# Optimization experiments

Measured on AMD Instinct MI355X. Metric: run time of the kernel, lower is better.

The kernel has to match this reference:

```python
import jax, jax.numpy as jnp
import numpy as np

D_MODEL = 1024
NUM_HEADS = 16
D_HEAD = D_MODEL // NUM_HEADS
THETA = 10000.0


def setup_inputs() -> dict:
    key = jax.random.key(0)
    ks = jax.random.split(key, 5)
    B, S = 2, 2048
    std = np.sqrt(2.0 / (D_MODEL + D_MODEL))
    return {
        "x": jax.random.normal(ks[0], (B, S, D_MODEL), dtype=jnp.float32),
        "token_positions": jnp.arange(S, dtype=jnp.int32),
        "wq": jax.random.normal(ks[1], (D_MODEL, D_MODEL), dtype=jnp.float32) * std,
        "wk": jax.random.normal(ks[2], (D_MODEL, D_MODEL), dtype=jnp.float32) * std,
        "wv": jax.random.normal(ks[3], (D_MODEL, D_MODEL), dtype=jnp.float32) * std,
        "wo": jax.random.normal(ks[4], (D_MODEL, D_MODEL), dtype=jnp.float32) * std,
    }


def _rope(x, token_positions):
    # x: [B, H, S, D_HEAD]; token_positions: [S]
    freq_idx = jnp.arange(0, D_HEAD, 2, dtype=jnp.float32)
    inv_freq = THETA ** (-freq_idx / D_HEAD)                      # [D_HEAD/2]
    angles = token_positions.astype(jnp.float32)[:, None] * inv_freq  # [S, D_HEAD/2]
    cos = jnp.cos(angles)[None, None, :, :]
    sin = jnp.sin(angles)[None, None, :, :]
    x_even = x[..., 0::2]
    x_odd = x[..., 1::2]
    rot_even = x_even * cos - x_odd * sin
    rot_odd = x_even * sin + x_odd * cos
    # interleave pairs back: [..., pairs, 2] -> [..., D_HEAD]
    return jnp.stack((rot_even, rot_odd), axis=-1).reshape(x.shape)


def reference(x, token_positions, wq, wk, wv, wo):
    B, S, _ = x.shape
    def proj(w):
        y = jnp.einsum('bsi,oi->bso', x, w)
        return y.reshape(B, S, NUM_HEADS, D_HEAD).transpose(0, 2, 1, 3)  # [B,H,S,Dh]
    q = _rope(proj(wq), token_positions)
    k = _rope(proj(wk), token_positions)
    v = proj(wv)
    scores = jnp.einsum('bhqd,bhkd->bhqk', q, k) / jnp.sqrt(jnp.float32(D_HEAD))
    causal = jnp.tril(jnp.ones((S, S), dtype=bool))
    scores = jnp.where(causal, scores, -jnp.inf)
    probs = jax.nn.softmax(scores, axis=-1)
    attn = jnp.einsum('bhqk,bhkd->bhqd', probs, v)
    attn = attn.transpose(0, 2, 1, 3).reshape(B, S, D_MODEL)
    return jnp.einsum('bsi,oi->bso', attn, wo)
```

## Files before the change

### kernel.cpp

```cpp
#include <hip/hip_runtime.h>
#include <math.h>

#define D_MODEL 1024
#define NUM_HEADS 16
#define D_HEAD 64
#define SEQ 2048
#define BATCH 2

typedef __attribute__((ext_vector_type(8))) short short8;
typedef __attribute__((ext_vector_type(4))) float float4v;

__device__ __forceinline__ short f2bf(float f) {
    unsigned u = __float_as_uint(f);
    u += 0x7FFFu + ((u >> 16) & 1u);
    return (short)(u >> 16);
}

__global__ __launch_bounds__(256) void cvt_bf16_kernel(
    const float* __restrict__ x,  const float* __restrict__ wq,
    const float* __restrict__ wk, const float* __restrict__ wv,
    const float* __restrict__ wo, const int* __restrict__ pos,
    short* __restrict__ xb,  short* __restrict__ wqb,
    short* __restrict__ wkb, short* __restrict__ wvb,
    short* __restrict__ wob,
    float* __restrict__ costab, float* __restrict__ sintab)
{
    const int a = blockIdx.y;
    if (a == 5) {
        const int idx = blockIdx.x * 256 + threadIdx.x;
        if (idx < SEQ * 32) {
            const int s = idx >> 5, fi = idx & 31;
            const float p = (float)pos[s];
            const float inv_freq = exp2f((float)fi * -0.4152410118609203f);
            float sn, cs;
            sincosf(p * inv_freq, &sn, &cs);
            costab[idx] = cs;
            sintab[idx] = sn;
        }
        return;
    }
    const float* src = (a == 0) ? x : (a == 1) ? wq : (a == 2) ? wk : (a == 3) ? wv : wo;
    short* dst = (a == 0) ? xb : (a == 1) ? wqb : (a == 2) ? wkb : (a == 3) ? wvb : wob;
    const int n = (a == 0) ? (BATCH * SEQ * D_MODEL) : (D_MODEL * D_MODEL);
    const int i = (blockIdx.x * 256 + threadIdx.x) * 8;
    if (i >= n) return;
    const float4 v0 = *(const float4*)(src + i);
    const float4 v1 = *(const float4*)(src + i + 4);
    short8 r;
    r[0] = f2bf(v0.x); r[1] = f2bf(v0.y); r[2] = f2bf(v0.z); r[3] = f2bf(v0.w);
    r[4] = f2bf(v1.x); r[5] = f2bf(v1.y); r[6] = f2bf(v1.z); r[7] = f2bf(v1.w);
    *(short8*)(dst + i) = r;
}

__device__ __forceinline__ void gemm_core_db(
    const short* __restrict__ a, const short* __restrict__ b,
    short* smem, int m0, int n0, float4v acc[4][4])
{
    const int tid = threadIdx.x;
    const int lane = tid & 63;
    const int l15 = lane & 15, quad = lane >> 4;
    const int wave = tid >> 6;
    const int mw = (wave & 1) * 64, nw = (wave >> 1) * 64;
    const int srow = tid >> 2;
    const int scol = (tid & 3) * 8;

    const short* ag = a + (size_t)(m0 + srow) * D_MODEL + scol;
    const short* bg = b + (size_t)(n0 + srow) * D_MODEL + scol;

    short* bufA[2] = { smem,        smem + 8192 };
    short* bufB[2] = { smem + 4096, smem + 12288 };

    short8 ga0 = *(const short8*)(ag);
    short8 ga1 = *(const short8*)(ag + (size_t)64 * D_MODEL);
    short8 gb0 = *(const short8*)(bg);
    short8 gb1 = *(const short8*)(bg + (size_t)64 * D_MODEL);
    *(short8*)&bufA[0][srow * 32 + scol]        = ga0;
    *(short8*)&bufA[0][(64 + srow) * 32 + scol] = ga1;
    *(short8*)&bufB[0][srow * 32 + scol]        = gb0;
    *(short8*)&bufB[0][(64 + srow) * 32 + scol] = gb1;
    ga0 = *(const short8*)(ag + 32);
    ga1 = *(const short8*)(ag + 32 + (size_t)64 * D_MODEL);
    gb0 = *(const short8*)(bg + 32);
    gb1 = *(const short8*)(bg + 32 + (size_t)64 * D_MODEL);

    for (int k = 0; k < 32; k++) {
        __syncthreads();
        if (k + 1 < 32) {
            short* bA = bufA[(k + 1) & 1];
            short* bB = bufB[(k + 1) & 1];
            *(short8*)&bA[srow * 32 + scol]        = ga0;
            *(short8*)&bA[(64 + srow) * 32 + scol] = ga1;
            *(short8*)&bB[srow * 32 + scol]        = gb0;
            *(short8*)&bB[(64 + srow) * 32 + scol] = gb1;
        }
        if (k + 2 < 32) {
            const int off = (k + 2) * 32;
            ga0 = *(const short8*)(ag + off);
            ga1 = *(const short8*)(ag + off + (size_t)64 * D_MODEL);
            gb0 = *(const short8*)(bg + off);
            gb1 = *(const short8*)(bg + off + (size_t)64 * D_MODEL);
        }
        const short* lA = bufA[k & 1];
        const short* lB = bufB[k & 1];
        short8 af[4], bf[4];
        #pragma unroll
        for (int i = 0; i < 4; i++)
            af[i] = *(const short8*)&lA[(mw + i * 16 + l15) * 32 + quad * 8];
        #pragma unroll
        for (int i = 0; i < 4; i++)
            bf[i] = *(const short8*)&lB[(nw + i * 16 + l15) * 32 + quad * 8];
        #pragma unroll
        for (int mi = 0; mi < 4; mi++)
            #pragma unroll
            for (int ni = 0; ni < 4; ni++)
                acc[mi][ni] = __builtin_amdgcn_mfma_f32_16x16x32_bf16(
                    af[mi], bf[ni], acc[mi][ni], 0, 0, 0);
    }
}

__global__ __launch_bounds__(256) void qk_mfma_kernel(
    const short* __restrict__ xb, const short* __restrict__ w,
    const float* __restrict__ costab, const float* __restrict__ sintab,
    short* __restrict__ dst, const float qs)
{
    __shared__ __align__(16) short smem[128 * 136];

    const int bid = blockIdx.x;
    const int m0 = (bid & 31) * 128;
    const int n0 = (bid >> 5) * 128;

    float4v acc[4][4];
    #pragma unroll
    for (int i = 0; i < 4; i++)
        #pragma unroll
        for (int j = 0; j < 4; j++)
            acc[i][j] = (float4v){0.f, 0.f, 0.f, 0.f};

    gemm_core_db(xb, w, smem, m0, n0, acc);

    const int tid = threadIdx.x;
    const int lane = tid & 63;
    const int l15 = lane & 15, quad = lane >> 4;
    const int wave = tid >> 6;
    const int mw = (wave & 1) * 64, nw = (wave >> 1) * 64;

    const int s_base = m0 & (SEQ - 1);
    const int bb = m0 >> 11;

    __syncthreads();

    #pragma unroll
    for (int ni = 0; ni < 4; ni++) {
        const int n = n0 + nw + ni * 16 + l15;
        const int d = n & 63;
        const int fi = d >> 1;
        #pragma unroll
        for (int mi = 0; mi < 4; mi++) {
            #pragma unroll
            for (int r = 0; r < 4; r++) {
                const int mloc = mw + mi * 16 + quad * 4 + r;
                const int ti = ((s_base + mloc) << 5) + fi;
                const float cs = costab[ti];
                const float sn = sintab[ti];
                const float val = acc[mi][ni][r];
                const float partner = __shfl_xor(val, 1, 64);
                const float res = (l15 & 1) ? fmaf(partner, sn, val * cs)
                                            : fmaf(val, cs, -partner * sn);
                smem[mloc * 136 + nw + ni * 16 + l15] = f2bf(res * qs);
            }
        }
    }
    __syncthreads();
    #pragma unroll
    for (int it = 0; it < 8; it++) {
        const int ri = it * 32 + (tid >> 3);
        const int mloc = ri & 127;
        const int hh = ri >> 7;
        const int nloc = hh * 64 + (tid & 7) * 8;
        const short8 val = *(const short8*)&smem[mloc * 136 + nloc];
        const int n = n0 + nloc;
        const int h = n >> 6, d = n & 63;
        *(short8*)(dst + ((size_t)(bb * NUM_HEADS + h) * SEQ + s_base + mloc) *
                   D_HEAD + d) = val;
    }
}

__global__ __launch_bounds__(256) void v_mfma_kernel(
    const short* __restrict__ xb, const short* __restrict__ w,
    short* __restrict__ Vt)
{
    __shared__ __align__(16) short smem[128 * 136];

    const int bid = blockIdx.x;
    const int m0 = (bid & 31) * 128;
    const int n0 = (bid >> 5) * 128;

    float4v acc[4][4];
    #pragma unroll
    for (int i = 0; i < 4; i++)
        #pragma unroll
        for (int j = 0; j < 4; j++)
            acc[i][j] = (float4v){0.f, 0.f, 0.f, 0.f};

    gemm_core_db(xb, w, smem, m0, n0, acc);

    const int tid = threadIdx.x;
    const int lane = tid & 63;
    const int l15 = lane & 15, quad = lane >> 4;
    const int wave = tid >> 6;
    const int mw = (wave & 1) * 64, nw = (wave >> 1) * 64;

    const int s_base = m0 & (SEQ - 1);
    const int bb = m0 >> 11;

    __syncthreads();
    #pragma unroll
    for (int ni = 0; ni < 4; ni++) {
        #pragma unroll
        for (int mi = 0; mi < 4; mi++) {
            #pragma unroll
            for (int r = 0; r < 4; r++)
                smem[(nw + ni * 16 + l15) * 136 + mw + mi * 16 + quad * 4 + r] =
                    f2bf(acc[mi][ni][r]);
        }
    }
    __syncthreads();
    #pragma unroll
    for (int it = 0; it < 8; it++) {
        const int nloc = it * 16 + (tid >> 4);
        const int mloc = (tid & 15) * 8;
        const short8 val = *(const short8*)&smem[nloc * 136 + mloc];
        const int n = n0 + nloc;
        const int h = n >> 6, d = n & 63;
        *(short8*)(Vt + ((size_t)(bb * NUM_HEADS + h) * D_HEAD + d) * SEQ +
                   s_base + mloc) = val;
    }
}

__global__ __launch_bounds__(256) void attn_mfma_kernel(
    const short* __restrict__ Qb, const short* __restrict__ Kb,
    const short* __restrict__ Vt, short* __restrict__ Ab)
{
    __shared__ __align__(16) short lK[32 * 72];
    __shared__ __align__(16) short lV[64 * 56];
    __shared__ __align__(16) short lP[4][16 * 56];

    const int tid = threadIdx.x;
    const int lane = tid & 63;
    const int wave = tid >> 6;
    const int l15 = lane & 15;
    const int quad = lane >> 4;

    const int bh = blockIdx.x & (BATCH * NUM_HEADS - 1);
    const int qt = (SEQ / 64 - 1) - (blockIdx.x >> 5);
    const int q0w = qt * 64 + wave * 16;

    const short* Kg = Kb + (size_t)bh * SEQ * D_HEAD;
    const short* Vg = Vt + (size_t)bh * D_HEAD * SEQ;

    const short* Qrow = Qb + ((size_t)bh * SEQ + q0w + l15) * D_HEAD;
    const short8 qf0 = *(const short8*)(Qrow + quad * 8);
    const short8 qf1 = *(const short8*)(Qrow + 32 + quad * 8);

    float4v o0 = {0.f, 0.f, 0.f, 0.f}, o1 = o0, o2 = o0, o3 = o0;
    float lp[4] = {0.f, 0.f, 0.f, 0.f};

    const int nt = qt * 2 + 2;
    const int krow = tid & 31, kch = tid >> 5;
    const int vrow = tid >> 2, vch = tid & 3;

    short8 kreg = *(const short8*)(Kg + (size_t)krow * D_HEAD + kch * 8);
    short8 vreg = *(const short8*)(Vg + (size_t)vrow * SEQ + vch * 8);

    for (int t = 0; t < nt; t++) {
        const int kt0 = t * 32;
        __syncthreads();
        *(short8*)&lK[krow * 72 + kch * 8] = kreg;
        *(short8*)&lV[vrow * 56 + vch * 8] = vreg;
        __syncthreads();
        if (t + 1 < nt) {
            kreg = *(const short8*)(Kg + (size_t)(kt0 + 32 + krow) * D_HEAD + kch * 8);
            vreg = *(const short8*)(Vg + (size_t)vrow * SEQ + kt0 + 32 + vch * 8);
        }
        if (kt0 > q0w + 15) continue;

        float4v s0 = {0.f, 0.f, 0.f, 0.f}, s1 = {0.f, 0.f, 0.f, 0.f};
        {
            const short8 b00 = *(const short8*)&lK[l15 * 72 + quad * 8];
            const short8 b10 = *(const short8*)&lK[(16 + l15) * 72 + quad * 8];
            s0 = __builtin_amdgcn_mfma_f32_16x16x32_bf16(qf0, b00, s0, 0, 0, 0);
            s1 = __builtin_amdgcn_mfma_f32_16x16x32_bf16(qf0, b10, s1, 0, 0, 0);
            const short8 b01 = *(const short8*)&lK[l15 * 72 + 32 + quad * 8];
            const short8 b11 = *(const short8*)&lK[(16 + l15) * 72 + 32 + quad * 8];
            s0 = __builtin_amdgcn_mfma_f32_16x16x32_bf16(qf1, b01, s0, 0, 0, 0);
            s1 = __builtin_amdgcn_mfma_f32_16x16x32_bf16(qf1, b11, s1, 0, 0, 0);
        }

        if (kt0 + 31 > q0w) {
            const int qbase = q0w + quad * 4;
            #pragma unroll
            for (int r = 0; r < 4; r++) {
                if (kt0 + l15 > qbase + r)      s0[r] = -INFINITY;
                if (kt0 + 16 + l15 > qbase + r) s1[r] = -INFINITY;
            }
        }

        float p0[4], p1[4];
        #pragma unroll
        for (int r = 0; r < 4; r++) {
            p0[r] = __expf(s0[r]);
            p1[r] = __expf(s1[r]);
            lp[r] += p0[r] + p1[r];
        }

        short* Pw = lP[wave];
        #pragma unroll
        for (int r = 0; r < 4; r++) {
            Pw[(quad * 4 + r) * 56 + l15]      = f2bf(p0[r]);
            Pw[(quad * 4 + r) * 56 + 16 + l15] = f2bf(p1[r]);
        }
        const short8 pa = *(const short8*)&lP[wave][l15 * 56 + quad * 8];

        const short8 v0 = *(const short8*)&lV[(0 * 16 + l15) * 56 + quad * 8];
        const short8 v1 = *(const short8*)&lV[(1 * 16 + l15) * 56 + quad * 8];
        const short8 v2 = *(const short8*)&lV[(2 * 16 + l15) * 56 + quad * 8];
        const short8 v3 = *(const short8*)&lV[(3 * 16 + l15) * 56 + quad * 8];
        o0 = __builtin_amdgcn_mfma_f32_16x16x32_bf16(pa, v0, o0, 0, 0, 0);
        o1 = __builtin_amdgcn_mfma_f32_16x16x32_bf16(pa, v1, o1, 0, 0, 0);
        o2 = __builtin_amdgcn_mfma_f32_16x16x32_bf16(pa, v2, o2, 0, 0, 0);
        o3 = __builtin_amdgcn_mfma_f32_16x16x32_bf16(pa, v3, o3, 0, 0, 0);
    }

    #pragma unroll
    for (int off = 1; off <= 8; off <<= 1) {
        #pragma unroll
        for (int r = 0; r < 4; r++) lp[r] += __shfl_xor(lp[r], off, 64);
    }

    const int b = bh >> 4, h = bh & 15;
    short* Ap = Ab + ((size_t)(b * SEQ) + q0w + quad * 4) * D_MODEL + h * D_HEAD;
    #pragma unroll
    for (int r = 0; r < 4; r++) {
        const float inv = 1.0f / lp[r];
        Ap[(size_t)r * D_MODEL + l15]      = f2bf(o0[r] * inv);
        Ap[(size_t)r * D_MODEL + 16 + l15] = f2bf(o1[r] * inv);
        Ap[(size_t)r * D_MODEL + 32 + l15] = f2bf(o2[r] * inv);
        Ap[(size_t)r * D_MODEL + 48 + l15] = f2bf(o3[r] * inv);
    }
}

__global__ __launch_bounds__(256) void out_mfma_kernel(
    const short* __restrict__ Ab, const short* __restrict__ wob,
    float* __restrict__ out)
{
    __shared__ __align__(16) short smem[2 * 8192];

    const int bid = blockIdx.x;
    const int m0 = (bid & 31) * 128;
    const int n0 = (bid >> 5) * 128;

    float4v acc[4][4];
    #pragma unroll
    for (int i = 0; i < 4; i++)
        #pragma unroll
        for (int j = 0; j < 4; j++)
            acc[i][j] = (float4v){0.f, 0.f, 0.f, 0.f};

    gemm_core_db(Ab, wob, smem, m0, n0, acc);

    const int tid = threadIdx.x;
    const int lane = tid & 63;
    const int l15 = lane & 15, quad = lane >> 4;
    const int wave = tid >> 6;
    const int mw = (wave & 1) * 64, nw = (wave >> 1) * 64;

    #pragma unroll
    for (int mi = 0; mi < 4; mi++) {
        #pragma unroll
        for (int r = 0; r < 4; r++) {
            const int m = m0 + mw + mi * 16 + quad * 4 + r;
            float* op = out + (size_t)m * D_MODEL + n0 + nw + l15;
            #pragma unroll
            for (int ni = 0; ni < 4; ni++)
                op[ni * 16] = acc[mi][ni][r];
        }
    }
}

extern "C" void kernel_launch(void* const* d_in, const int* in_sizes, int n_in,
                              void* d_out, int out_size, void* d_ws, size_t ws_size,
                              hipStream_t stream)
{
    const float* x  = (const float*)d_in[0];
    const int*  pos = (const int*)d_in[1];
    const float* wq = (const float*)d_in[2];
    const float* wk = (const float*)d_in[3];
    const float* wv = (const float*)d_in[4];
    const float* wo = (const float*)d_in[5];
    float* out = (float*)d_out;

    const size_t nx = (size_t)BATCH * SEQ * D_MODEL;
    const size_t nw = (size_t)D_MODEL * D_MODEL;
    short* xb  = (short*)d_ws;
    short* wqb = xb + nx;
    short* wkb = wqb + nw;
    short* wvb = wkb + nw;
    short* wob = wvb + nw;
    short* Qb  = wob + nw;
    short* Kb  = Qb + nx;
    short* Vt  = Kb + nx;
    short* Ab  = Vt + nx;
    float* costab = (float*)(Ab + nx);
    float* sintab = costab + SEQ * 32;

    dim3 blk(256);
    cvt_bf16_kernel<<<dim3(2048, 6), blk, 0, stream>>>(x, wq, wk, wv, wo, pos,
                                                       xb, wqb, wkb, wvb, wob,
                                                       costab, sintab);
    qk_mfma_kernel<<<dim3(256), blk, 0, stream>>>(xb, wqb, costab, sintab, Qb, 0.125f);
    qk_mfma_kernel<<<dim3(256), blk, 0, stream>>>(xb, wkb, costab, sintab, Kb, 1.0f);
    v_mfma_kernel<<<dim3(256), blk, 0, stream>>>(xb, wvb, Vt);
    attn_mfma_kernel<<<dim3(BATCH * NUM_HEADS * (SEQ / 64)), blk, 0, stream>>>(Qb, Kb, Vt, Ab);
    out_mfma_kernel<<<dim3(256), blk, 0, stream>>>(Ab, wob, out);
}
```

Before: 213.1 us.

## Merge Q/K/V projections into one launch and widen attention key tiles to 64

The three projection launches (Q, K with RoPE; V transposed) become a single 768-block kernel that picks its weight and epilogue by block index. This removes launch gaps and fills the GPU better than three 256-block grids. The attention kernel now processes 64 keys per iteration instead of 32 and computes S transposed (K as the A operand), so each lane owns one query row. That lets it keep a single running row sum, write P as packed 4-short stores and apply the causal mask through a predicated exp. The cost is more shared memory per block and more work per iteration on diagonal tiles, since whole 64-key tiles are processed even when partly masked.

```diff
diff --git a/kernel.cpp b/kernel.cpp
--- a/kernel.cpp
+++ b/kernel.cpp
@@ -8,6 +8,7 @@
 #define BATCH 2
 
 typedef __attribute__((ext_vector_type(8))) short short8;
+typedef __attribute__((ext_vector_type(4))) short short4v;
 typedef __attribute__((ext_vector_type(4))) float float4v;
 
 __device__ __forceinline__ short f2bf(float f) {
@@ -118,16 +119,19 @@
     }
 }
 
-__global__ __launch_bounds__(256) void qk_mfma_kernel(
-    const short* __restrict__ xb, const short* __restrict__ w,
+__global__ __launch_bounds__(256) void qkv_mfma_kernel(
+    const short* __restrict__ xb, const short* __restrict__ wqb,
+    const short* __restrict__ wkb, const short* __restrict__ wvb,
     const float* __restrict__ costab, const float* __restrict__ sintab,
-    short* __restrict__ dst, const float qs)
+    short* __restrict__ Qb, short* __restrict__ Kb, short* __restrict__ Vt)
 {
     __shared__ __align__(16) short smem[128 * 136];
 
-    const int bid = blockIdx.x;
+    const int z = blockIdx.x >> 8;
+    const int bid = blockIdx.x & 255;
     const int m0 = (bid & 31) * 128;
     const int n0 = (bid >> 5) * 128;
+    const short* w = (z == 0) ? wqb : (z == 1) ? wkb : wvb;
 
     float4v acc[4][4];
     #pragma unroll
@@ -143,97 +147,70 @@
     const int l15 = lane & 15, quad = lane >> 4;
     const int wave = tid >> 6;
     const int mw = (wave & 1) * 64, nw = (wave >> 1) * 64;
-
     const int s_base = m0 & (SEQ - 1);
     const int bb = m0 >> 11;
 
     __syncthreads();
 
-    #pragma unroll
-    for (int ni = 0; ni < 4; ni++) {
-        const int n = n0 + nw + ni * 16 + l15;
-        const int d = n & 63;
-        const int fi = d >> 1;
-        #pragma unroll
-        for (int mi = 0; mi < 4; mi++) {
+    if (z == 2) {
+        #pragma unroll
+        for (int ni = 0; ni < 4; ni++) {
             #pragma unroll
-            for (int r = 0; r < 4; r++) {
-                const int mloc = mw + mi * 16 + quad * 4 + r;
-                const int ti = ((s_base + mloc) << 5) + fi;
-                const float cs = costab[ti];
-                const float sn = sintab[ti];
-                const float val = acc[mi][ni][r];
-                const float partner = __shfl_xor(val, 1, 64);
-                const float res = (l15 & 1) ? fmaf(partner, sn, val * cs)
-                                            : fmaf(val, cs, -partner * sn);
-                smem[mloc * 136 + nw + ni * 16 + l15] = f2bf(res * qs);
+            for (int mi = 0; mi < 4; mi++) {
+                #pragma unroll
+                for (int r = 0; r < 4; r++)
+                    smem[(nw + ni * 16 + l15) * 136 + mw + mi * 16 + quad * 4 + r] =
+                        f2bf(acc[mi][ni][r]);
             }
         }
-    }
-    __syncthreads();
-    #pragma unroll
-    for (int it = 0; it < 8; it++) {
-        const int ri = it * 32 + (tid >> 3);
-        const int mloc = ri & 127;
-        const int hh = ri >> 7;
-        const int nloc = hh * 64 + (tid & 7) * 8;
-        const short8 val = *(const short8*)&smem[mloc * 136 + nloc];
-        const int n = n0 + nloc;
-        const int h = n >> 6, d = n & 63;
-        *(short8*)(dst + ((size_t)(bb * NUM_HEADS + h) * SEQ + s_base + mloc) *
-                   D_HEAD + d) = val;
-    }
-}
-
-__global__ __launch_bounds__(256) void v_mfma_kernel(
-    const short* __restrict__ xb, const short* __restrict__ w,
-    short* __restrict__ Vt)
-{
-    __shared__ __align__(16) short smem[128 * 136];
-
-    const int bid = blockIdx.x;
-    const int m0 = (bid & 31) * 128;
-    const int n0 = (bid >> 5) * 128;
-
-    float4v acc[4][4];
-    #pragma unroll
-    for (int i = 0; i < 4; i++)
-        #pragma unroll
-        for (int j = 0; j < 4; j++)
-            acc[i][j] = (float4v){0.f, 0.f, 0.f, 0.f};
-
-    gemm_core_db(xb, w, smem, m0, n0, acc);
-
-    const int tid = threadIdx.x;
-    const int lane = tid & 63;
-    const int l15 = lane & 15, quad = lane >> 4;
-    const int wave = tid >> 6;
-    const int mw = (wave & 1) * 64, nw = (wave >> 1) * 64;
-
-    const int s_base = m0 & (SEQ - 1);
-    const int bb = m0 >> 11;
-
-    __syncthreads();
-    #pragma unroll
-    for (int ni = 0; ni < 4; ni++) {
-        #pragma unroll
-        for (int mi = 0; mi < 4; mi++) {
+        __syncthreads();
+        #pragma unroll
+        for (int it = 0; it < 8; it++) {
+            const int nloc = it * 16 + (tid >> 4);
+            const int mloc = (tid & 15) * 8;
+            const short8 val = *(const short8*)&smem[nloc * 136 + mloc];
+            const int n = n0 + nloc;
+            const int h = n >> 6, d = n & 63;
+            *(short8*)(Vt + ((size_t)(bb * NUM_HEADS + h) * D_HEAD + d) * SEQ +
+                       s_base + mloc) = val;
+        }
+    } else {
+        short* dst = (z == 0) ? Qb : Kb;
+        const float qs = (z == 0) ? 0.125f : 1.0f;
+        #pragma unroll
+        for (int ni = 0; ni < 4; ni++) {
+            const int n = n0 + nw + ni * 16 + l15;
+            const int d = n & 63;
+            const int fi = d >> 1;
             #pragma unroll
-            for (int r = 0; r < 4; r++)
-                smem[(nw + ni * 16 + l15) * 136 + mw + mi * 16 + quad * 4 + r] =
-                    f2bf(acc[mi][ni][r]);
-        }
-    }
-    __syncthreads();
-    #pragma unroll
-    for (int it = 0; it < 8; it++) {
-        const int nloc = it * 16 + (tid >> 4);
-        const int mloc = (tid & 15) * 8;
-        const short8 val = *(const short8*)&smem[nloc * 136 + mloc];
-        const int n = n0 + nloc;
-        const int h = n >> 6, d = n & 63;
-        *(short8*)(Vt + ((size_t)(bb * NUM_HEADS + h) * D_HEAD + d) * SEQ +
-                   s_base + mloc) = val;
+            for (int mi = 0; mi < 4; mi++) {
+                #pragma unroll
+                for (int r = 0; r < 4; r++) {
+                    const int mloc = mw + mi * 16 + quad * 4 + r;
+                    const int ti = ((s_base + mloc) << 5) + fi;
+                    const float cs = costab[ti];
+                    const float sn = sintab[ti];
+                    const float val = acc[mi][ni][r];
+                    const float partner = __shfl_xor(val, 1, 64);
+                    const float res = (l15 & 1) ? fmaf(partner, sn, val * cs)
+                                                : fmaf(val, cs, -partner * sn);
+                    smem[mloc * 136 + nw + ni * 16 + l15] = f2bf(res * qs);
+                }
+            }
+        }
+        __syncthreads();
+        #pragma unroll
+        for (int it = 0; it < 8; it++) {
+            const int ri = it * 32 + (tid >> 3);
+            const int mloc = ri & 127;
+            const int hh = ri >> 7;
+            const int nloc = hh * 64 + (tid & 7) * 8;
+            const short8 val = *(const short8*)&smem[mloc * 136 + nloc];
+            const int n = n0 + nloc;
+            const int h = n >> 6, d = n & 63;
+            *(short8*)(dst + ((size_t)(bb * NUM_HEADS + h) * SEQ + s_base + mloc) *
+                       D_HEAD + d) = val;
+        }
     }
 }
 
@@ -241,9 +218,9 @@
     const short* __restrict__ Qb, const short* __restrict__ Kb,
     const short* __restrict__ Vt, short* __restrict__ Ab)
 {
-    __shared__ __align__(16) short lK[32 * 72];
-    __shared__ __align__(16) short lV[64 * 56];
-    __shared__ __align__(16) short lP[4][16 * 56];
+    __shared__ __align__(16) short lK[64 * 72];
+    __shared__ __align__(16) short lV[64 * 72];
+    __shared__ __align__(16) short lP[4][16 * 72];
 
     const int tid = threadIdx.x;
     const int lane = tid & 63;
@@ -254,6 +231,7 @@
     const int bh = blockIdx.x & (BATCH * NUM_HEADS - 1);
     const int qt = (SEQ / 64 - 1) - (blockIdx.x >> 5);
     const int q0w = qt * 64 + wave * 16;
+    const int qcmp = q0w + l15;
 
     const short* Kg = Kb + (size_t)bh * SEQ * D_HEAD;
     const short* Vg = Vt + (size_t)bh * D_HEAD * SEQ;
@@ -263,85 +241,89 @@
     const short8 qf1 = *(const short8*)(Qrow + 32 + quad * 8);
 
     float4v o0 = {0.f, 0.f, 0.f, 0.f}, o1 = o0, o2 = o0, o3 = o0;
-    float lp[4] = {0.f, 0.f, 0.f, 0.f};
-
-    const int nt = qt * 2 + 2;
-    const int krow = tid & 31, kch = tid >> 5;
-    const int vrow = tid >> 2, vch = tid & 3;
-
-    short8 kreg = *(const short8*)(Kg + (size_t)krow * D_HEAD + kch * 8);
-    short8 vreg = *(const short8*)(Vg + (size_t)vrow * SEQ + vch * 8);
+    float lp = 0.f;
+
+    const int nt = qt + 1;
+    const int srow = tid >> 2;
+    const int sch = (tid & 3) * 8;
+
+    short8 k0 = *(const short8*)(Kg + (size_t)srow * D_HEAD + sch);
+    short8 k1 = *(const short8*)(Kg + (size_t)srow * D_HEAD + sch + 32);
+    short8 v0 = *(const short8*)(Vg + (size_t)srow * SEQ + sch);
+    short8 v1 = *(const short8*)(Vg + (size_t)srow * SEQ + sch + 32);
 
     for (int t = 0; t < nt; t++) {
-        const int kt0 = t * 32;
+        const int kt0 = t * 64;
         __syncthreads();
-        *(short8*)&lK[krow * 72 + kch * 8] = kreg;
-        *(short8*)&lV[vrow * 56 + vch * 8] = vreg;
+        *(short8*)&lK[srow * 72 + sch]      = k0;
+        *(short8*)&lK[srow * 72 + sch + 32] = k1;
+        *(short8*)&lV[srow * 72 + sch]      = v0;
+        *(short8*)&lV[srow * 72 + sch + 32] = v1;
         __syncthreads();
         if (t + 1 < nt) {
-            kreg = *(const short8*)(Kg + (size_t)(kt0 + 32 + krow) * D_HEAD + kch * 8);
-            vreg = *(const short8*)(Vg + (size_t)vrow * SEQ + kt0 + 32 + vch * 8);
-        }
-        if (kt0 > q0w + 15) continue;
-
-        float4v s0 = {0.f, 0.f, 0.f, 0.f}, s1 = {0.f, 0.f, 0.f, 0.f};
-        {
-            const short8 b00 = *(const short8*)&lK[l15 * 72 + quad * 8];
-            const short8 b10 = *(const short8*)&lK[(16 + l15) * 72 + quad * 8];
-            s0 = __builtin_amdgcn_mfma_f32_16x16x32_bf16(qf0, b00, s0, 0, 0, 0);
-            s1 = __builtin_amdgcn_mfma_f32_16x16x32_bf16(qf0, b10, s1, 0, 0, 0);
-            const short8 b01 = *(const short8*)&lK[l15 * 72 + 32 + quad * 8];
-            const short8 b11 = *(const short8*)&lK[(16 + l15) * 72 + 32 + quad * 8];
-            s0 = __builtin_amdgcn_mfma_f32_16x16x32_bf16(qf1, b01, s0, 0, 0, 0);
-            s1 = __builtin_amdgcn_mfma_f32_16x16x32_bf16(qf1, b11, s1, 0, 0, 0);
-        }
-
-        if (kt0 + 31 > q0w) {
-            const int qbase = q0w + quad * 4;
+            k0 = *(const short8*)(Kg + (size_t)(kt0 + 64 + srow) * D_HEAD + sch);
+            k1 = *(const short8*)(Kg + (size_t)(kt0 + 64 + srow) * D_HEAD + sch + 32);
+            v0 = *(const short8*)(Vg + (size_t)srow * SEQ + kt0 + 64 + sch);
+            v1 = *(const short8*)(Vg + (size_t)srow * SEQ + kt0 + 64 + sch + 32);
+        }
+
+        short* Pw = lP[wave];
+        #pragma unroll
+        for (int g = 0; g < 4; g++) {
+            float4v s = {0.f, 0.f, 0.f, 0.f};
+            const short8 ka = *(const short8*)&lK[(g * 16 + l15) * 72 + quad * 8];
+            s = __builtin_amdgcn_mfma_f32_16x16x32_bf16(ka, qf0, s, 0, 0, 0);
+            const short8 kb = *(const short8*)&lK[(g * 16 + l15) * 72 + 32 + quad * 8];
+            s = __builtin_amdgcn_mfma_f32_16x16x32_bf16(kb, qf1, s, 0, 0, 0);
+
+            const int kbase = kt0 + g * 16 + quad * 4;
+            short4v pk;
             #pragma unroll
             for (int r = 0; r < 4; r++) {
-                if (kt0 + l15 > qbase + r)      s0[r] = -INFINITY;
-                if (kt0 + 16 + l15 > qbase + r) s1[r] = -INFINITY;
+                const float e = (kbase + r <= qcmp) ? __expf(s[r]) : 0.f;
+                lp += e;
+                pk[r] = f2bf(e);
             }
-        }
-
-        float p0[4], p1[4];
-        #pragma unroll
-        for (int r = 0; r < 4; r++) {
-            p0[r] = __expf(s0[r]);
-            p1[r] = __expf(s1[r]);
-            lp[r] += p0[r] + p1[r];
-        }
-
-        short* Pw = lP[wave];
-        #pragma unroll
-        for (int r = 0; r < 4; r++) {
-            Pw[(quad * 4 + r) * 56 + l15]      = f2bf(p0[r]);
-            Pw[(quad * 4 + r) * 56 + 16 + l15] = f2bf(p1[r]);
-        }
-        const short8 pa = *(const short8*)&lP[wave][l15 * 56 + quad * 8];
-
-        const short8 v0 = *(const short8*)&lV[(0 * 16 + l15) * 56 + quad * 8];
-        const short8 v1 = *(const short8*)&lV[(1 * 16 + l15) * 56 + quad * 8];
-        const short8 v2 = *(const short8*)&lV[(2 * 16 + l15) * 56 + quad * 8];
-        const short8 v3 = *(const short8*)&lV[(3 * 16 + l15) * 56 + quad * 8];
-        o0 = __builtin_amdgcn_mfma_f32_16x16x32_bf16(pa, v0, o0, 0, 0, 0);
-        o1 = __builtin_amdgcn_mfma_f32_16x16x32_bf16(pa, v1, o1, 0, 0, 0);
-        o2 = __builtin_amdgcn_mfma_f32_16x16x32_bf16(pa, v2, o2, 0, 0, 0);
-        o3 = __builtin_amdgcn_mfma_f32_16x16x32_bf16(pa, v3, o3, 0, 0, 0);
-    }
-
-    #pragma unroll
-    for (int off = 1; off <= 8; off <<= 1) {
-        #pragma unroll
-        for (int r = 0; r < 4; r++) lp[r] += __shfl_xor(lp[r], off, 64);
-    }
+            *(short4v*)&Pw[l15 * 72 + g * 16 + quad * 4] = pk;
+        }
+
+        const short8 pa0 = *(const short8*)&lP[wave][l15 * 72 + quad * 8];
+        const short8 pa1 = *(const short8*)&lP[wave][l15 * 72 + 32 + quad * 8];
+
+        {
+            const short8 va = *(const short8*)&lV[(0 * 16 + l15) * 72 + quad * 8];
+            const short8 vb = *(const short8*)&lV[(0 * 16 + l15) * 72 + 32 + quad * 8];
+            o0 = __builtin_amdgcn_mfma_f32_16x16x32_bf16(pa0, va, o0, 0, 0, 0);
+            o0 = __builtin_amdgcn_mfma_f32_16x16x32_bf16(pa1, vb, o0, 0, 0, 0);
+        }
+        {
+            const short8 va = *(const short8*)&lV[(1 * 16 + l15) * 72 + quad * 8];
+            const short8 vb = *(const short8*)&lV[(1 * 16 + l15) * 72 + 32 + quad * 8];
+            o1 = __builtin_amdgcn_mfma_f32_16x16x32_bf16(pa0, va, o1, 0, 0, 0);
+            o1 = __builtin_amdgcn_mfma_f32_16x16x32_bf16(pa1, vb, o1, 0, 0, 0);
+        }
+        {
+            const short8 va = *(const short8*)&lV[(2 * 16 + l15) * 72 + quad * 8];
+            const short8 vb = *(const short8*)&lV[(2 * 16 + l15) * 72 + 32 + quad * 8];
+            o2 = __builtin_amdgcn_mfma_f32_16x16x32_bf16(pa0, va, o2, 0, 0, 0);
+            o2 = __builtin_amdgcn_mfma_f32_16x16x32_bf16(pa1, vb, o2, 0, 0, 0);
+        }
+        {
+            const short8 va = *(const short8*)&lV[(3 * 16 + l15) * 72 + quad * 8];
+            const short8 vb = *(const short8*)&lV[(3 * 16 + l15) * 72 + 32 + quad * 8];
+            o3 = __builtin_amdgcn_mfma_f32_16x16x32_bf16(pa0, va, o3, 0, 0, 0);
+            o3 = __builtin_amdgcn_mfma_f32_16x16x32_bf16(pa1, vb, o3, 0, 0, 0);
+        }
+    }
+
+    lp += __shfl_xor(lp, 16, 64);
+    lp += __shfl_xor(lp, 32, 64);
 
     const int b = bh >> 4, h = bh & 15;
     short* Ap = Ab + ((size_t)(b * SEQ) + q0w + quad * 4) * D_MODEL + h * D_HEAD;
     #pragma unroll
     for (int r = 0; r < 4; r++) {
-        const float inv = 1.0f / lp[r];
+        const float inv = 1.0f / __shfl(lp, quad * 4 + r, 64);
         Ap[(size_t)r * D_MODEL + l15]      = f2bf(o0[r] * inv);
         Ap[(size_t)r * D_MODEL + 16 + l15] = f2bf(o1[r] * inv);
         Ap[(size_t)r * D_MODEL + 32 + l15] = f2bf(o2[r] * inv);
@@ -417,9 +399,8 @@
     cvt_bf16_kernel<<<dim3(2048, 6), blk, 0, stream>>>(x, wq, wk, wv, wo, pos,
                                                        xb, wqb, wkb, wvb, wob,
                                                        costab, sintab);
-    qk_mfma_kernel<<<dim3(256), blk, 0, stream>>>(xb, wqb, costab, sintab, Qb, 0.125f);
-    qk_mfma_kernel<<<dim3(256), blk, 0, stream>>>(xb, wkb, costab, sintab, Kb, 1.0f);
-    v_mfma_kernel<<<dim3(256), blk, 0, stream>>>(xb, wvb, Vt);
+    qkv_mfma_kernel<<<dim3(768), blk, 0, stream>>>(xb, wqb, wkb, wvb,
+                                                   costab, sintab, Qb, Kb, Vt);
     attn_mfma_kernel<<<dim3(BATCH * NUM_HEADS * (SEQ / 64)), blk, 0, stream>>>(Qb, Kb, Vt, Ab);
     out_mfma_kernel<<<dim3(256), blk, 0, stream>>>(Ab, wob, out);
 }
```

Result: faster. 187.8 us (-11.9%).
